# Kernel tuning notes

Measured on AMD Instinct MI355X. Metric: run time of the kernel, lower is better.

The kernel has to match this reference:

```python
import jax, jax.numpy as jnp
import numpy as np

B, N, C = 32, 1025, 768
H, D = 12, 64          # num_heads, head_dim
M = 4 * D              # num random features = 256
HEIGHT, WIDTH = 32, 32 # spatial grid; N = HEIGHT*WIDTH + 1 (CLS)
EPS = 1e-6


def setup_inputs() -> dict:
    key = jax.random.key(0)
    ks = jax.random.split(key, 7)
    x = jax.random.normal(ks[0], (B, N, C), jnp.float32)
    w_qkv = jax.random.normal(ks[1], (3 * C, C), jnp.float32) * 0.02
    w_proj = jax.random.normal(ks[2], (C, C), jnp.float32) * 0.02
    b_proj = jnp.zeros((C,), jnp.float32)
    c_row = jax.random.normal(ks[3], (H, D), jnp.float32) * 0.02
    c_col = jax.random.normal(ks[4], (H, D), jnp.float32) * 0.02
    # orthogonal random-feature projection (m, d): QR blocks scaled by chi norm
    blocks = []
    for i in range(M // D):
        Hm = jax.random.normal(jax.random.fold_in(ks[5], i), (D, D), jnp.float32)
        Q, _ = jnp.linalg.qr(Hm)
        nrm = jnp.linalg.norm(jax.random.normal(jax.random.fold_in(ks[6], i), (D,), jnp.float32))
        blocks.append(Q * nrm)
    proj_feat = jnp.concatenate(blocks, axis=0)  # (M, D)
    return {"x": x, "w_qkv": w_qkv, "w_proj": w_proj, "b_proj": b_proj,
            "c_row": c_row, "c_col": c_col, "proj_feat": proj_feat}


def _string(xp, c_row, c_col):
    """Circulant-STRING rotation. xp: (B,H,Np,D)."""
    rows = jnp.arange(HEIGHT, dtype=jnp.float32)
    cols = jnp.arange(WIDTH, dtype=jnp.float32)
    gr, gc = jnp.meshgrid(rows, cols, indexing='ij')
    pos_r = gr.ravel()  # (Np,)
    pos_c = gc.ravel()
    # g: (H, Np, D)
    g = pos_r[None, :, None] * c_row[:, None, :] + pos_c[None, :, None] * c_col[:, None, :]
    g_fft = jnp.fft.fft(g, axis=-1)
    exp_lambda = jnp.exp(2j * g_fft.imag)          # (H, Np, D) complex, unit modulus
    x_fft = jnp.fft.fft(xp, axis=-1)               # (B, H, Np, D) complex
    rotated = jnp.fft.ifft(exp_lambda[None] * x_fft, axis=-1).real
    return rotated.astype(xp.dtype)


def _favor(x, proj):
    """Positive random feature map. x: (B,H,N,D), proj: (M,D) -> (B,H,N,M)."""
    xs = x * (D ** -0.25)
    px = jnp.einsum('bhnd,md->bhnm', xs, proj)
    norm_sq = 0.5 * jnp.sum(xs * xs, axis=-1, keepdims=True)
    return jnp.exp(px - norm_sq)


def reference(x, w_qkv, w_proj, b_proj, c_row, c_col, proj_feat):
    qkv = x @ w_qkv.T                                  # (B, N, 3C)
    qkv = qkv.reshape(B, N, 3, H, D).transpose(2, 0, 3, 1, 4)  # (3,B,H,N,D)
    q, k, v = qkv[0], qkv[1], qkv[2]
    # N == HEIGHT*WIDTH + 1 -> CLS token at position 0 is left unrotated
    q_cls, q_p = q[:, :, :1, :], q[:, :, 1:, :]
    k_cls, k_p = k[:, :, :1, :], k[:, :, 1:, :]
    q = jnp.concatenate([q_cls, _string(q_p, c_row, c_col)], axis=2)
    k = jnp.concatenate([k_cls, _string(k_p, c_row, c_col)], axis=2)
    q_feat = _favor(q, proj_feat)                      # (B,H,N,M)
    k_feat = _favor(k, proj_feat)
    # bidirectional linear attention
    context = jnp.einsum('bhnm,bhne->bhme', k_feat, v) # (B,H,M,D)
    num = jnp.einsum('bhnm,bhme->bhne', q_feat, context)
    k_sum = k_feat.sum(axis=2)                         # (B,H,M)
    den = jnp.einsum('bhnm,bhm->bhn', q_feat, k_sum)[..., None]
    den = jnp.maximum(den, EPS)
    out = num / den                                    # (B,H,N,D)
    out = out.transpose(0, 2, 1, 3).reshape(B, N, C)
    return out @ w_proj.T + b_proj
```

## Files before the change

kernel.cpp:

```cpp
#include <hip/hip_runtime.h>
#include <math.h>

typedef _Float16 f16;
typedef _Float16 f16x8 __attribute__((ext_vector_type(8)));
typedef _Float16 f16x4 __attribute__((ext_vector_type(4)));
typedef float f32x4 __attribute__((ext_vector_type(4)));

#define LDSK 40
#define NTOK 1025
#define CC 768
#define HH 12
#define DD 64
#define MM 256
#define VPAD 1056
#define BN_ROWS 32800

__device__ __forceinline__ void load_row16(const f16* p, f16x8& a0, f16x8& a1) {
    a0 = *(const f16x8*)p;
    a1 = *(const f16x8*)(p + 8);
}
__device__ __forceinline__ void load_row16(const float* p, f16x8& a0, f16x8& a1) {
    const float4* q = (const float4*)p;
    float4 u0 = q[0], u1 = q[1], u2 = q[2], u3 = q[3];
    a0[0] = (f16)u0.x; a0[1] = (f16)u0.y; a0[2] = (f16)u0.z; a0[3] = (f16)u0.w;
    a0[4] = (f16)u1.x; a0[5] = (f16)u1.y; a0[6] = (f16)u1.z; a0[7] = (f16)u1.w;
    a1[0] = (f16)u2.x; a1[1] = (f16)u2.y; a1[2] = (f16)u2.z; a1[3] = (f16)u2.w;
    a1[4] = (f16)u3.x; a1[5] = (f16)u3.y; a1[6] = (f16)u3.z; a1[7] = (f16)u3.w;
}

__device__ __forceinline__ void gload16(const f16* g, f16* l) {
    __builtin_amdgcn_global_load_lds(
        (const __attribute__((address_space(1))) unsigned int*)g,
        (__attribute__((address_space(3))) unsigned int*)l, 16, 0, 0);
}

__global__ void k_diag(float* out, float v) {
    if (threadIdx.x == 0 && blockIdx.x == 0) out[0] = v;
}

__global__ __launch_bounds__(256) void k_cvt_x(const float* __restrict__ x, f16* __restrict__ xw) {
    size_t i = ((size_t)blockIdx.x * 256 + threadIdx.x) * 4;
    float4 v;
    if (i < (size_t)BN_ROWS * CC) v = *(const float4*)(x + i);
    else v = make_float4(0.f, 0.f, 0.f, 0.f);
    f16x4 o; o[0] = (f16)v.x; o[1] = (f16)v.y; o[2] = (f16)v.z; o[3] = (f16)v.w;
    *(f16x4*)(xw + i) = o;
}

__global__ __launch_bounds__(256) void k_cvt(const float* __restrict__ in, f16* __restrict__ out,
                                             long n, float scale) {
    long i = (long)blockIdx.x * 256 + threadIdx.x;
    if (i < n) out[i] = (f16)(in[i] * scale);
}

__global__ __launch_bounds__(256) void k_zpad(f16* __restrict__ v16t) {
    int bh = blockIdx.x;
    for (int u = threadIdx.x; u < 64 * 31; u += 256) {
        int d = u / 31, j = u - d * 31;
        v16t[((size_t)bh * DD + d) * VPAD + 1025 + j] = (f16)0.f;
    }
}

__global__ __launch_bounds__(64) void k_ab(const float* __restrict__ c_row,
                                           const float* __restrict__ c_col,
                                           float* __restrict__ ab) {
    int h = blockIdx.x, k = threadIdx.x;
    float sa = 0.f, sb = 0.f;
    for (int d = 0; d < 64; ++d) {
        float s = sinf((float)((k * d) & 63) * (6.283185307179586f / 64.f));
        sa += c_row[h * 64 + d] * s;
        sb += c_col[h * 64 + d] * s;
    }
    ab[h * 64 + k] = -2.f * sa;
    ab[768 + h * 64 + k] = -2.f * sb;
}

__global__ __launch_bounds__(64) void k_wcirc(const float* __restrict__ ab, float* __restrict__ wc) {
    int hp = blockIdx.x; int h = hp >> 10; int p = hp & 1023;
    float pr = (float)(p >> 5), pc = (float)(p & 31);
    int t = threadIdx.x;
    __shared__ float th[64];
    th[t] = pr * ab[h * 64 + t] + pc * ab[768 + h * 64 + t];
    __syncthreads();
    float s = 0.f;
    #pragma unroll 8
    for (int k = 0; k < 64; ++k) {
        float arg = th[k] + (float)((k * t) & 63) * (6.283185307179586f / 64.f);
        s += __cosf(arg);
    }
    wc[(size_t)hp * 64 + t] = s * (1.f / 64.f);
}

template <bool GA, typename TA, typename TB>
__device__ __forceinline__ void gemm128_core(const TA* __restrict__ A, const TB* __restrict__ Bm,
                                             int K, int row0, int col0, int Alim,
                                             f32x4 (&acc)[4][4],
                                             f16 (*As)[LDSK], f16 (*Bs)[LDSK]) {
    const int tid = threadIdx.x;
    const int lane = tid & 63;
    const int lr = tid >> 1, lk = (tid & 1) * 16;
    const int frow = lane & 15, fk = (lane >> 4) * 8;
    const int wave = tid >> 6, wr = wave >> 1, wc = wave & 1;
    for (int kt = 0; kt < K; kt += 32) {
        f16x8 a0 = {}, a1 = {}, b0, b1;
        if (!GA || (row0 + lr) < Alim)
            load_row16(A + (size_t)(row0 + lr) * K + kt + lk, a0, a1);
        load_row16(Bm + (size_t)(col0 + lr) * K + kt + lk, b0, b1);
        __syncthreads();
        *(f16x8*)&As[lr][lk] = a0; *(f16x8*)&As[lr][lk + 8] = a1;
        *(f16x8*)&Bs[lr][lk] = b0; *(f16x8*)&Bs[lr][lk + 8] = b1;
        __syncthreads();
        f16x8 af[4], bf[4];
        #pragma unroll
        for (int m = 0; m < 4; ++m) af[m] = *(const f16x8*)&As[wr * 64 + m * 16 + frow][fk];
        #pragma unroll
        for (int n = 0; n < 4; ++n) bf[n] = *(const f16x8*)&Bs[wc * 64 + n * 16 + frow][fk];
        #pragma unroll
        for (int m = 0; m < 4; ++m)
            #pragma unroll
            for (int n = 0; n < 4; ++n)
                acc[m][n] = __builtin_amdgcn_mfma_f32_16x16x32_f16(af[m], bf[n], acc[m][n], 0, 0, 0);
    }
}

__device__ __forceinline__ void gemm128_pipe(const f16* __restrict__ A, const f16* __restrict__ Bm,
                                             int K, int row0, int col0,
                                             f32x4 (&acc)[4][4], f16* As, f16* Bs) {
    const int tid = threadIdx.x;
    const int lane = tid & 63, wave = tid >> 6;
    const int frow = lane & 15, fk8 = (lane >> 4) * 8;
    const int wr = wave >> 1, wc = wave & 1;
    const int srow = lane >> 3;
    const int scol = ((lane & 7) ^ srow) * 8;
    const f16* aG = A + (size_t)(row0 + wave * 32 + srow) * K + scol;
    const f16* bG = Bm + (size_t)(col0 + wave * 32 + srow) * K + scol;
    const int aoff = (wave * 32) * 64;
    const int cswz = (frow & 7) * 8;
    #pragma unroll
    for (int j = 0; j < 4; ++j) {
        gload16(aG + (size_t)(8 * j) * K, As + aoff + (8 * j) * 64);
        gload16(bG + (size_t)(8 * j) * K, Bs + aoff + (8 * j) * 64);
    }
    int cur = 0;
    for (int kt = 0; kt < K; kt += 64) {
        asm volatile("s_waitcnt vmcnt(0)" ::: "memory");
        __builtin_amdgcn_s_barrier();
        asm volatile("" ::: "memory");
        if (kt + 64 < K) {
            int nb = (cur ^ 1) * 8192;
            #pragma unroll
            for (int j = 0; j < 4; ++j) {
                gload16(aG + kt + 64 + (size_t)(8 * j) * K, As + nb + aoff + (8 * j) * 64);
                gload16(bG + kt + 64 + (size_t)(8 * j) * K, Bs + nb + aoff + (8 * j) * 64);
            }
        }
        const f16* Ac = As + cur * 8192;
        const f16* Bc = Bs + cur * 8192;
        #pragma unroll
        for (int ks = 0; ks < 2; ++ks) {
            f16x8 af[4], bf[4];
            #pragma unroll
            for (int m = 0; m < 4; ++m)
                af[m] = *(const f16x8*)&Ac[(wr * 64 + m * 16 + frow) * 64 + ((ks * 32 + fk8) ^ cswz)];
            #pragma unroll
            for (int n = 0; n < 4; ++n)
                bf[n] = *(const f16x8*)&Bc[(wc * 64 + n * 16 + frow) * 64 + ((ks * 32 + fk8) ^ cswz)];
            #pragma unroll
            for (int m = 0; m < 4; ++m)
                #pragma unroll
                for (int n = 0; n < 4; ++n)
                    acc[m][n] = __builtin_amdgcn_mfma_f32_16x16x32_f16(af[m], bf[n], acc[m][n], 0, 0, 0);
        }
        cur ^= 1;
    }
}

__device__ __forceinline__ void qkv_epilogue(f32x4 (&acc)[4][4], int row0, int col0,
                                             f16* __restrict__ q16, f16* __restrict__ k16,
                                             f16* __restrict__ v16t) {
    int lane = threadIdx.x & 63, wave = threadIdx.x >> 6;
    int wr = wave >> 1, wc = wave & 1;
    int rb = row0 + wr * 64 + 4 * (lane >> 4);
    int cb = col0 + wc * 64 + (lane & 15);
    #pragma unroll
    for (int m = 0; m < 4; ++m)
        #pragma unroll
        for (int n = 0; n < 4; ++n)
            #pragma unroll
            for (int i = 0; i < 4; ++i) {
                int r = rb + m * 16 + i;
                if (r >= BN_ROWS) continue;
                int j = cb + n * 16;
                int b = r / NTOK, nn = r - b * NTOK;
                int t = j / CC, rem = j - t * CC;
                int h = rem >> 6, d = rem & 63;
                size_t bh = (size_t)b * HH + h;
                f16 val = (f16)acc[m][n][i];
                if (t == 0) q16[(bh * NTOK + nn) * DD + d] = val;
                else if (t == 1) k16[(bh * NTOK + nn) * DD + d] = val;
                else v16t[(bh * DD + d) * VPAD + nn] = val;
            }
}

__global__ __launch_bounds__(256) void k_gemm_qkv_dma(const f16* __restrict__ A, const f16* __restrict__ Bm,
                                                      f16* __restrict__ q16, f16* __restrict__ k16,
                                                      f16* __restrict__ v16t) {
    __shared__ __attribute__((aligned(16))) f16 As[2 * 128 * 64];
    __shared__ __attribute__((aligned(16))) f16 Bs[2 * 128 * 64];
    const int q = 578, r = 2;
    int xg = blockIdx.x & 7, o8 = blockIdx.x >> 3;
    int wg = (xg < r ? xg * (q + 1) : r * (q + 1) + (xg - r) * q) + o8;
    int row0 = (wg / 18) * 128, col0 = (wg % 18) * 128;
    f32x4 acc[4][4] = {};
    gemm128_pipe(A, Bm, CC, row0, col0, acc, As, Bs);
    qkv_epilogue(acc, row0, col0, q16, k16, v16t);
}

__global__ __launch_bounds__(256) void k_gemm_qkv_f32(const float* __restrict__ A, const f16* __restrict__ Bm,
                                                      f16* __restrict__ q16, f16* __restrict__ k16,
                                                      f16* __restrict__ v16t) {
    __shared__ __attribute__((aligned(16))) f16 As[128][LDSK];
    __shared__ __attribute__((aligned(16))) f16 Bs[128][LDSK];
    f32x4 acc[4][4] = {};
    int row0 = blockIdx.x * 128, col0 = blockIdx.y * 128;
    gemm128_core<true>(A, Bm, CC, row0, col0, BN_ROWS, acc, As, Bs);
    qkv_epilogue(acc, row0, col0, q16, k16, v16t);
}

__global__ __launch_bounds__(256) void k_rotate(const float* __restrict__ wcirc,
                                                f16* __restrict__ q16, f16* __restrict__ k16,
                                                float* __restrict__ nsqq, float* __restrict__ nsqk) {
    const int p = blockIdx.x, h = blockIdx.y;
    const int nn = p + 1;
    const int tid = threadIdx.x;
    __shared__ float wl[64];
    __shared__ __attribute__((aligned(16))) f16 Ws[64][72];
    __shared__ __attribute__((aligned(16))) f16 Xs[64][72];
    if (tid < 64) wl[tid] = wcirc[((size_t)h * 1024 + p) * 64 + tid];
    {
        const int row = tid >> 2;
        const int ch = (tid & 3) * 16;
        const int b = row & 31;
        const f16* src = ((row < 32) ? q16 : k16) + (((size_t)b * HH + h) * NTOK + nn) * DD + ch;
        f16x8 v0 = *(const f16x8*)src;
        f16x8 v1 = *(const f16x8*)(src + 8);
        *(f16x8*)&Xs[row][ch] = v0;
        *(f16x8*)&Xs[row][ch + 8] = v1;
    }
    __syncthreads();
    #pragma unroll
    for (int j = 0; j < 16; ++j) {
        int idx = tid * 16 + j;
        int d = idx >> 6, m = idx & 63;
        Ws[d][m] = (f16)wl[(d - m) & 63];
    }
    __syncthreads();
    const int lane = tid & 63, wave = tid >> 6;
    const int frow = lane & 15, fk = (lane >> 4) * 8;
    f32x4 acc[4] = {};
    #pragma unroll
    for (int kt = 0; kt < 64; kt += 32) {
        f16x8 a = *(const f16x8*)&Xs[wave * 16 + frow][kt + fk];
        #pragma unroll
        for (int n = 0; n < 4; ++n) {
            f16x8 bfr = *(const f16x8*)&Ws[n * 16 + frow][kt + fk];
            acc[n] = __builtin_amdgcn_mfma_f32_16x16x32_f16(a, bfr, acc[n], 0, 0, 0);
        }
    }
    #pragma unroll
    for (int i = 0; i < 4; ++i) {
        int row = wave * 16 + 4 * (lane >> 4) + i;
        int b = row & 31;
        f16* dst = ((row < 32) ? q16 : k16) + (((size_t)b * HH + h) * NTOK + nn) * DD;
        float ss = 0.f;
        #pragma unroll
        for (int n = 0; n < 4; ++n) {
            float v = acc[n][i];
            dst[n * 16 + (lane & 15)] = (f16)v;
            ss += v * v;
        }
        ss += __shfl_xor(ss, 1); ss += __shfl_xor(ss, 2);
        ss += __shfl_xor(ss, 4); ss += __shfl_xor(ss, 8);
        if ((lane & 15) == 0) {
            float* nd = (row < 32) ? nsqq : nsqk;
            nd[((size_t)b * HH + h) * NTOK + nn] = ss * (1.f / 16.f);
        }
    }
}

__global__ __launch_bounds__(256) void k_cls_nsq(const f16* __restrict__ q16, const f16* __restrict__ k16,
                                                 float* __restrict__ nsqq, float* __restrict__ nsqk) {
    int gw = (blockIdx.x * 256 + threadIdx.x) >> 6;
    int lane = threadIdx.x & 63;
    int which = gw & 1; int bh = gw >> 1;
    const f16* src = (which ? k16 : q16) + (size_t)bh * NTOK * DD;
    float v = (float)src[lane];
    float ss = v * v;
    for (int off = 1; off < 64; off <<= 1) ss += __shfl_xor(ss, off);
    if (lane == 0) (which ? nsqk : nsqq)[(size_t)bh * NTOK] = ss * (1.f / 16.f);
}

__global__ __launch_bounds__(512) void k_fctx(const f16* __restrict__ k16, const f16* __restrict__ v16t,
                                              const f16* __restrict__ pfeat, const float* __restrict__ nsqk,
                                              f16* __restrict__ ctxT) {
    __shared__ __attribute__((aligned(16))) f16 uLDS[80 * 136];
    f16 (*fts)[LDSK] = (f16(*)[LDSK])uLDS;
    f16 (*cx)[136]   = (f16(*)[136])uLDS;
    const int bh = blockIdx.x;
    const int tid = threadIdx.x;
    const int lane = tid & 63, w = tid >> 6;
    const int frow = lane & 15, fk8 = (lane >> 4) * 8;
    const int m0 = w * 32;
    f16x8 pf[2][2];
    #pragma unroll
    for (int mf = 0; mf < 2; ++mf)
        #pragma unroll
        for (int kf = 0; kf < 2; ++kf)
            pf[mf][kf] = *(const f16x8*)&pfeat[(m0 + mf * 16 + frow) * DD + kf * 32 + fk8];
    const f16* kb_base = k16 + (size_t)bh * NTOK * DD;
    const f16* vb_base = v16t + (size_t)bh * DD * VPAD;
    const float* ns_base = nsqk + (size_t)bh * NTOK;
    auto loadK = [&](f16x8 (&kb)[2][2], int n0) {
        #pragma unroll
        for (int nf = 0; nf < 2; ++nf) {
            int n = n0 + nf * 16 + frow;
            #pragma unroll
            for (int kf = 0; kf < 2; ++kf) {
                f16x8 z = {};
                if (n < NTOK) z = *(const f16x8*)&kb_base[(size_t)n * DD + kf * 32 + fk8];
                kb[nf][kf] = z;
            }
        }
    };
    f32x4 acc[2][5] = {};
    f16x8 kb[2][2];
    loadK(kb, 0);
    for (int n0 = 0; n0 < VPAD; n0 += 32) {
        f16x8 vb[4];
        #pragma unroll
        for (int ef = 0; ef < 4; ++ef)
            vb[ef] = *(const f16x8*)&vb_base[(size_t)(ef * 16 + frow) * VPAD + n0 + fk8];
        f32x4 fa[2][2] = {};
        #pragma unroll
        for (int kf = 0; kf < 2; ++kf)
            #pragma unroll
            for (int mf = 0; mf < 2; ++mf)
                #pragma unroll
                for (int nf = 0; nf < 2; ++nf)
                    fa[mf][nf] = __builtin_amdgcn_mfma_f32_16x16x32_f16(pf[mf][kf], kb[nf][kf], fa[mf][nf], 0, 0, 0);
        f16x8 kbn[2][2];
        loadK(kbn, n0 + 32);
        #pragma unroll
        for (int nf = 0; nf < 2; ++nf) {
            int ncol = n0 + nf * 16 + frow;
            float ns = (ncol < NTOK) ? ns_base[ncol] : 0.f;
            #pragma unroll
            for (int mf = 0; mf < 2; ++mf)
                #pragma unroll
                for (int i = 0; i < 4; ++i) {
                    int mloc = m0 + mf * 16 + 4 * (lane >> 4) + i;
                    float v = (ncol < NTOK) ? fminf(__expf(fa[mf][nf][i] - ns), 60000.f) : 0.f;
                    fts[mloc][nf * 16 + frow] = (f16)v;
                }
        }
        __syncthreads();
        f16x8 afr[2];
        #pragma unroll
        for (int mf = 0; mf < 2; ++mf) afr[mf] = *(const f16x8*)&fts[m0 + mf * 16 + frow][fk8];
        #pragma unroll
        for (int ef = 0; ef < 4; ++ef)
            #pragma unroll
            for (int mf = 0; mf < 2; ++mf)
                acc[mf][ef] = __builtin_amdgcn_mfma_f32_16x16x32_f16(afr[mf], vb[ef], acc[mf][ef], 0, 0, 0);
        {
            f16x8 bfr;
            #pragma unroll
            for (int j = 0; j < 8; ++j)
                bfr[j] = (f16)((frow == 0 && (n0 + fk8 + j) < NTOK) ? 1.f : 0.f);
            #pragma unroll
            for (int mf = 0; mf < 2; ++mf)
                acc[mf][4] = __builtin_amdgcn_mfma_f32_16x16x32_f16(afr[mf], bfr, acc[mf][4], 0, 0, 0);
        }
        __syncthreads();
        #pragma unroll
        for (int nf = 0; nf < 2; ++nf)
            #pragma unroll
            for (int kf = 0; kf < 2; ++kf)
                kb[nf][kf] = kbn[nf][kf];
    }
    #pragma unroll
    for (int p = 0; p < 2; ++p) {
        __syncthreads();
        if ((w >> 2) == p) {
            int mb = m0 - p * 128;
            #pragma unroll
            for (int mf = 0; mf < 2; ++mf)
                #pragma unroll
                for (int ef = 0; ef < 5; ++ef) {
                    int e = ef * 16 + frow;
                    f16x4 pk;
                    #pragma unroll
                    for (int i = 0; i < 4; ++i) pk[i] = (f16)acc[mf][ef][i];
                    *(f16x4*)&cx[e][mb + mf * 16 + 4 * (lane >> 4)] = pk;
                }
        }
        __syncthreads();
        for (int u = tid; u < 80 * 16; u += 512) {
            int e = u >> 4, seg = u & 15;
            *(f16x8*)&ctxT[((size_t)bh * 80 + e) * MM + p * 128 + seg * 8] =
                *(const f16x8*)&cx[e][seg * 8];
        }
    }
}

__global__ __launch_bounds__(256) void k_fnum(const f16* __restrict__ q16, const f16* __restrict__ pfeat,
                                              const float* __restrict__ nsqq, const f16* __restrict__ ctxT,
                                              f16* __restrict__ attn) {
    __shared__ __attribute__((aligned(16))) f16 qf_s[128][72];
    const int bh = blockIdx.y;
    const int b = bh / HH, h = bh - b * HH;
    const int t0 = blockIdx.x * 128;
    const int tid = threadIdx.x;
    const int lane = tid & 63, w = tid >> 6;
    const int frow = lane & 15, fk8 = (lane >> 4) * 8;
    const f16* qbase = q16 + (size_t)bh * NTOK * DD;
    const f16* cbase = ctxT + (size_t)bh * 80 * MM;
    f16x8 qa[2][2];
    float ns[2][4];
    #pragma unroll
    for (int tf = 0; tf < 2; ++tf) {
        int t = t0 + w * 32 + tf * 16 + frow;
        #pragma unroll
        for (int kf = 0; kf < 2; ++kf) {
            f16x8 z = {};
            if (t < NTOK) z = *(const f16x8*)&qbase[(size_t)t * DD + kf * 32 + fk8];
            qa[tf][kf] = z;
        }
        #pragma unroll
        for (int i = 0; i < 4; ++i) {
            int tr = t0 + w * 32 + tf * 16 + 4 * (lane >> 4) + i;
            ns[tf][i] = (tr < NTOK) ? nsqq[(size_t)bh * NTOK + tr] : 0.f;
        }
    }
    auto loadPB = [&](f16x8 (&pb)[2][2], int mc) {
        #pragma unroll
        for (int nf = 0; nf < 2; ++nf)
            #pragma unroll
            for (int kf = 0; kf < 2; ++kf)
                pb[nf][kf] = *(const f16x8*)&pfeat[(mc * 32 + nf * 16 + frow) * DD + kf * 32 + fk8];
    };
    f32x4 acc[2][5] = {};
    f16x8 pb[2][2];
    loadPB(pb, 0);
    #pragma unroll
    for (int mc = 0; mc < 8; ++mc) {
        f32x4 fa[2][2] = {};
        #pragma unroll
        for (int kf = 0; kf < 2; ++kf)
            #pragma unroll
            for (int tf = 0; tf < 2; ++tf)
                #pragma unroll
                for (int nf = 0; nf < 2; ++nf)
                    fa[tf][nf] = __builtin_amdgcn_mfma_f32_16x16x32_f16(qa[tf][kf], pb[nf][kf], fa[tf][nf], 0, 0, 0);
        f16x8 pbn[2][2];
        loadPB(pbn, (mc + 1) & 7);
        #pragma unroll
        for (int tf = 0; tf < 2; ++tf)
            #pragma unroll
            for (int nf = 0; nf < 2; ++nf)
                #pragma unroll
                for (int i = 0; i < 4; ++i) {
                    int tl = w * 32 + tf * 16 + 4 * (lane >> 4) + i;
                    float v = fminf(__expf(fa[tf][nf][i] - ns[tf][i]), 60000.f);
                    qf_s[tl][nf * 16 + frow] = (f16)v;
                }
        __syncthreads();
        f16x8 afr[2];
        #pragma unroll
        for (int tf = 0; tf < 2; ++tf) afr[tf] = *(const f16x8*)&qf_s[w * 32 + tf * 16 + frow][fk8];
        #pragma unroll
        for (int ef = 0; ef < 5; ++ef) {
            f16x8 bfr = *(const f16x8*)&cbase[(size_t)(ef * 16 + frow) * MM + mc * 32 + fk8];
            #pragma unroll
            for (int tf = 0; tf < 2; ++tf)
                acc[tf][ef] = __builtin_amdgcn_mfma_f32_16x16x32_f16(afr[tf], bfr, acc[tf][ef], 0, 0, 0);
        }
        __syncthreads();
        #pragma unroll
        for (int nf = 0; nf < 2; ++nf)
            #pragma unroll
            for (int kf = 0; kf < 2; ++kf)
                pb[nf][kf] = pbn[nf][kf];
    }
    #pragma unroll
    for (int tf = 0; tf < 2; ++tf)
        #pragma unroll
        for (int i = 0; i < 4; ++i) {
            float den = fmaxf(__shfl(acc[tf][4][i], lane & 48), 1e-6f);
            int tl = w * 32 + tf * 16 + 4 * (lane >> 4) + i;
            #pragma unroll
            for (int ef = 0; ef < 4; ++ef)
                qf_s[tl][ef * 16 + frow] = (f16)(acc[tf][ef][i] / den);
        }
    __syncthreads();
    for (int u = tid; u < 128 * 8; u += 256) {
        int tok = u >> 3, seg = u & 7;
        if (t0 + tok < NTOK)
            *(f16x8*)&attn[((size_t)(b * NTOK + t0 + tok)) * CC + h * DD + seg * 8] =
                *(const f16x8*)&qf_s[tok][seg * 8];
    }
}

__device__ __forceinline__ void proj_epilogue(f32x4 (&acc)[4][4], int row0, int col0,
                                              const float* __restrict__ bias, float* __restrict__ out) {
    int lane = threadIdx.x & 63, wave = threadIdx.x >> 6;
    int wr = wave >> 1, wc = wave & 1;
    int rb = row0 + wr * 64 + 4 * (lane >> 4);
    int cb = col0 + wc * 64 + (lane & 15);
    #pragma unroll
    for (int n = 0; n < 4; ++n) {
        int j = cb + n * 16;
        float bj = bias[j];
        #pragma unroll
        for (int m = 0; m < 4; ++m)
            #pragma unroll
            for (int i = 0; i < 4; ++i) {
                int r = rb + m * 16 + i;
                if (r < BN_ROWS) out[(size_t)r * CC + j] = acc[m][n][i] + bj;
            }
    }
}

__global__ __launch_bounds__(256) void k_gemm_proj_dma(const f16* __restrict__ A, const f16* __restrict__ Bm,
                                                       const float* __restrict__ bias, float* __restrict__ out) {
    __shared__ __attribute__((aligned(16))) f16 As[2 * 128 * 64];
    __shared__ __attribute__((aligned(16))) f16 Bs[2 * 128 * 64];
    const int q = 192, r = 6;
    int xg = blockIdx.x & 7, o8 = blockIdx.x >> 3;
    int wg = (xg < r ? xg * (q + 1) : r * (q + 1) + (xg - r) * q) + o8;
    int row0 = (wg / 6) * 128, col0 = (wg % 6) * 128;
    f32x4 acc[4][4] = {};
    gemm128_pipe(A, Bm, CC, row0, col0, acc, As, Bs);
    proj_epilogue(acc, row0, col0, bias, out);
}

__global__ __launch_bounds__(256) void k_gemm_proj(const f16* __restrict__ A, const f16* __restrict__ Bm,
                                                   const float* __restrict__ bias, float* __restrict__ out) {
    __shared__ __attribute__((aligned(16))) f16 As[128][LDSK];
    __shared__ __attribute__((aligned(16))) f16 Bs[128][LDSK];
    f32x4 acc[4][4] = {};
    int row0 = blockIdx.x * 128, col0 = blockIdx.y * 128;
    gemm128_core<true>(A, Bm, CC, row0, col0, BN_ROWS, acc, As, Bs);
    proj_epilogue(acc, row0, col0, bias, out);
}

extern "C" void kernel_launch(void* const* d_in, const int* in_sizes, int n_in,
                              void* d_out, int out_size, void* d_ws, size_t ws_size,
                              hipStream_t stream) {
    const float* x = (const float*)d_in[0];
    const float* w_qkv = (const float*)d_in[1];
    const float* w_proj = (const float*)d_in[2];
    const float* b_proj = (const float*)d_in[3];
    const float* c_row = (const float*)d_in[4];
    const float* c_col = (const float*)d_in[5];
    const float* proj_feat = (const float*)d_in[6];
    float* out = (float*)d_out;
    char* ws = (char*)d_ws;
    char* ob = (char*)d_out;

    const size_t O_WQKV  = 0;
    const size_t O_WPROJ = 3538944;
    const size_t O_Q16   = 4718592;
    const size_t O_K16   = 55099392;
    const size_t O_XW    = 105480192;
    const size_t NEED_B  = 105480192;
    const size_t NEED_A  = 156008448;
    if (ws_size < NEED_B) {
        k_diag<<<1, 64, 0, stream>>>(out, (float)((double)ws_size / 1048576.0));
        return;
    }
    const bool useA = (ws_size >= NEED_A);

    const size_t OD_V    = 0;
    const size_t OD_CTX  = 51904512;
    const size_t OD_WC   = 67633152;
    const size_t OD_NSQQ = 70778880;
    const size_t OD_NSQK = 72353280;
    const size_t OD_PF   = 73927680;
    const size_t OD_AB   = 73960448;

    f16* wqkv16  = (f16*)(ws + O_WQKV);
    f16* wproj16 = (f16*)(ws + O_WPROJ);
    f16* q16     = (f16*)(ws + O_Q16);
    f16* k16     = (f16*)(ws + O_K16);
    f16* xw16    = (f16*)(ws + O_XW);
    f16* v16t    = (f16*)(ob + OD_V);
    f16* ctxT    = (f16*)(ob + OD_CTX);
    float* wcirc = (float*)(ob + OD_WC);
    float* nsqq  = (float*)(ob + OD_NSQQ);
    float* nsqk  = (float*)(ob + OD_NSQK);
    f16* pfeat16 = (f16*)(ob + OD_PF);
    float* ab    = (float*)(ob + OD_AB);
    f16* attn16  = k16;

    k_cvt<<<6912, 256, 0, stream>>>(w_qkv, wqkv16, 1769472L, 1.f);
    k_cvt<<<2304, 256, 0, stream>>>(w_proj, wproj16, 589824L, 1.f);
    k_cvt<<<64, 256, 0, stream>>>(proj_feat, pfeat16, 16384L, 0.3535533906f);
    k_ab<<<12, 64, 0, stream>>>(c_row, c_col, ab);
    k_wcirc<<<12288, 64, 0, stream>>>(ab, wcirc);

    if (useA) {
        k_cvt_x<<<24672, 256, 0, stream>>>(x, xw16);
        k_gemm_qkv_dma<<<4626, 256, 0, stream>>>(xw16, wqkv16, q16, k16, v16t);
    } else {
        k_gemm_qkv_f32<<<dim3(257, 18), 256, 0, stream>>>(x, wqkv16, q16, k16, v16t);
    }
    k_zpad<<<384, 256, 0, stream>>>(v16t);

    k_rotate<<<dim3(1024, 12), 256, 0, stream>>>(wcirc, q16, k16, nsqq, nsqk);
    k_cls_nsq<<<192, 256, 0, stream>>>(q16, k16, nsqq, nsqk);

    k_fctx<<<384, 512, 0, stream>>>(k16, v16t, pfeat16, nsqk, ctxT);
    k_fnum<<<dim3(9, 384), 256, 0, stream>>>(q16, pfeat16, nsqq, ctxT, attn16);

    if (useA) {
        k_gemm_proj_dma<<<1542, 256, 0, stream>>>(attn16, wproj16, b_proj, out);
    } else {
        k_gemm_proj<<<dim3(257, 6), 256, 0, stream>>>(attn16, wproj16, b_proj, out);
    }

    (void)in_sizes; (void)n_in; (void)out_size;
}
```

Before: 658.8 us.

## Enlarge QKV and projection GEMM tiles to 256x256 with 512-thread blocks

Replaces the 128x128 pipelined GEMM with a 256x256-tile version using 8 waves per block, each wave computing 128x64 with an 8x4 MFMA accumulator array. K is fixed at 768 and the loop is fully specialised, with out-of-range A rows clamped instead of padded. Larger tiles raise arithmetic intensity and cut global/LDS traffic per FLOP, but use 128KB of LDS and more registers, which limits occupancy and makes the last row tile more wasteful. The epilogues are restructured to compute head/type indexing once per lane.

```diff
diff --git a/kernel.cpp b/kernel.cpp
--- a/kernel.cpp
+++ b/kernel.cpp
@@ -123,56 +123,132 @@
     }
 }
 
-__device__ __forceinline__ void gemm128_pipe(const f16* __restrict__ A, const f16* __restrict__ Bm,
-                                             int K, int row0, int col0,
-                                             f32x4 (&acc)[4][4], f16* As, f16* Bs) {
+__device__ __forceinline__ void gemm256_pipe(const f16* __restrict__ A, const f16* __restrict__ Bm,
+                                             int row0, int col0, int aclamp,
+                                             f32x4 (&acc)[8][4], f16* As, f16* Bs) {
     const int tid = threadIdx.x;
-    const int lane = tid & 63, wave = tid >> 6;
-    const int frow = lane & 15, fk8 = (lane >> 4) * 8;
-    const int wr = wave >> 1, wc = wave & 1;
+    const int lane = tid & 63, w = tid >> 6;
+    const int frow = lane & 15;
     const int srow = lane >> 3;
-    const int scol = ((lane & 7) ^ srow) * 8;
-    const f16* aG = A + (size_t)(row0 + wave * 32 + srow) * K + scol;
-    const f16* bG = Bm + (size_t)(col0 + wave * 32 + srow) * K + scol;
-    const int aoff = (wave * 32) * 64;
+    const int schk = ((lane & 7) ^ srow) * 8;
+    const f16* aG[4]; const f16* bG[4];
+    f16* aL[4]; f16* bL[4];
+    #pragma unroll
+    for (int j = 0; j < 4; ++j) {
+        int ra = row0 + w * 32 + 8 * j + srow;
+        if (ra > aclamp) ra = aclamp;
+        aG[j] = A + (size_t)ra * CC + schk;
+        bG[j] = Bm + (size_t)(col0 + w * 32 + 8 * j + srow) * CC + schk;
+        aL[j] = As + (w * 32 + 8 * j) * 64;
+        bL[j] = Bs + (w * 32 + 8 * j) * 64;
+    }
+    auto STAGE = [&](int tt) {
+        int bo = (tt & 1) * 16384, ko = tt * 64;
+        #pragma unroll
+        for (int j = 0; j < 4; ++j) {
+            gload16(aG[j] + ko, aL[j] + bo);
+            gload16(bG[j] + ko, bL[j] + bo);
+        }
+    };
+    STAGE(0);
+    const int wr = w >> 2, wcn = w & 3;
+    const int fk8 = (lane >> 4) * 8;
     const int cswz = (frow & 7) * 8;
-    #pragma unroll
-    for (int j = 0; j < 4; ++j) {
-        gload16(aG + (size_t)(8 * j) * K, As + aoff + (8 * j) * 64);
-        gload16(bG + (size_t)(8 * j) * K, Bs + aoff + (8 * j) * 64);
-    }
-    int cur = 0;
-    for (int kt = 0; kt < K; kt += 64) {
+    for (int t = 0; t < 12; ++t) {
         asm volatile("s_waitcnt vmcnt(0)" ::: "memory");
         __builtin_amdgcn_s_barrier();
-        asm volatile("" ::: "memory");
-        if (kt + 64 < K) {
-            int nb = (cur ^ 1) * 8192;
-            #pragma unroll
-            for (int j = 0; j < 4; ++j) {
-                gload16(aG + kt + 64 + (size_t)(8 * j) * K, As + nb + aoff + (8 * j) * 64);
-                gload16(bG + kt + 64 + (size_t)(8 * j) * K, Bs + nb + aoff + (8 * j) * 64);
+        __builtin_amdgcn_sched_barrier(0);
+        if (t < 11) STAGE(t + 1);
+        const f16* Ac = As + (t & 1) * 16384;
+        const f16* Bc = Bs + (t & 1) * 16384;
+        #pragma unroll
+        for (int ks = 0; ks < 2; ++ks) {
+            const int co = (ks * 32 + fk8) ^ cswz;
+            f16x8 af[8], bf[4];
+            #pragma unroll
+            for (int n = 0; n < 4; ++n)
+                bf[n] = *(const f16x8*)&Bc[(wcn * 64 + n * 16 + frow) * 64 + co];
+            #pragma unroll
+            for (int m = 0; m < 8; ++m)
+                af[m] = *(const f16x8*)&Ac[(wr * 128 + m * 16 + frow) * 64 + co];
+            #pragma unroll
+            for (int n = 0; n < 4; ++n)
+                #pragma unroll
+                for (int m = 0; m < 8; ++m)
+                    acc[m][n] = __builtin_amdgcn_mfma_f32_16x16x32_f16(af[m], bf[n], acc[m][n], 0, 0, 0);
+        }
+    }
+}
+
+__global__ __launch_bounds__(512, 2) void k_gemm_qkv_256(const f16* __restrict__ A, const f16* __restrict__ Bm,
+                                                         f16* __restrict__ q16, f16* __restrict__ k16,
+                                                         f16* __restrict__ v16t) {
+    __shared__ __attribute__((aligned(16))) f16 As[2 * 256 * 64];
+    __shared__ __attribute__((aligned(16))) f16 Bs[2 * 256 * 64];
+    const int q = 145, r = 1;
+    int xg = blockIdx.x & 7, o8 = blockIdx.x >> 3;
+    int wg = (xg < r ? xg * (q + 1) : r * (q + 1) + (xg - r) * q) + o8;
+    int row0 = (wg / 9) * 256, col0 = (wg % 9) * 256;
+    f32x4 acc[8][4] = {};
+    gemm256_pipe(A, Bm, row0, col0, 32895, acc, As, Bs);
+    const int lane = threadIdx.x & 63, w = threadIdx.x >> 6;
+    const int wr = w >> 2, wcn = w & 3;
+    int cb = col0 + wcn * 64 + (lane & 15);
+    int tt = cb / CC;
+    int h = (cb - tt * CC) >> 6;
+    int d0 = lane & 15;
+    int rb = row0 + wr * 128 + 4 * (lane >> 4);
+    #pragma unroll
+    for (int m = 0; m < 8; ++m)
+        #pragma unroll
+        for (int i = 0; i < 4; ++i) {
+            int rr = rb + m * 16 + i;
+            if (rr >= BN_ROWS) continue;
+            int b = rr / NTOK, nn = rr - b * NTOK;
+            size_t bh = (size_t)b * HH + h;
+            if (tt == 0) {
+                f16* p = q16 + (bh * NTOK + nn) * DD + d0;
+                #pragma unroll
+                for (int n = 0; n < 4; ++n) p[n * 16] = (f16)acc[m][n][i];
+            } else if (tt == 1) {
+                f16* p = k16 + (bh * NTOK + nn) * DD + d0;
+                #pragma unroll
+                for (int n = 0; n < 4; ++n) p[n * 16] = (f16)acc[m][n][i];
+            } else {
+                f16* p = v16t + (bh * DD + d0) * VPAD + nn;
+                #pragma unroll
+                for (int n = 0; n < 4; ++n) p[(size_t)n * 16 * VPAD] = (f16)acc[m][n][i];
             }
         }
-        const f16* Ac = As + cur * 8192;
-        const f16* Bc = Bs + cur * 8192;
-        #pragma unroll
-        for (int ks = 0; ks < 2; ++ks) {
-            f16x8 af[4], bf[4];
-            #pragma unroll
-            for (int m = 0; m < 4; ++m)
-                af[m] = *(const f16x8*)&Ac[(wr * 64 + m * 16 + frow) * 64 + ((ks * 32 + fk8) ^ cswz)];
-            #pragma unroll
-            for (int n = 0; n < 4; ++n)
-                bf[n] = *(const f16x8*)&Bc[(wc * 64 + n * 16 + frow) * 64 + ((ks * 32 + fk8) ^ cswz)];
-            #pragma unroll
-            for (int m = 0; m < 4; ++m)
-                #pragma unroll
-                for (int n = 0; n < 4; ++n)
-                    acc[m][n] = __builtin_amdgcn_mfma_f32_16x16x32_f16(af[m], bf[n], acc[m][n], 0, 0, 0);
-        }
-        cur ^= 1;
-    }
+}
+
+__global__ __launch_bounds__(512, 2) void k_gemm_proj_256(const f16* __restrict__ A, const f16* __restrict__ Bm,
+                                                          const float* __restrict__ bias, float* __restrict__ out) {
+    __shared__ __attribute__((aligned(16))) f16 As[2 * 256 * 64];
+    __shared__ __attribute__((aligned(16))) f16 Bs[2 * 256 * 64];
+    const int q = 48, r = 3;
+    int xg = blockIdx.x & 7, o8 = blockIdx.x >> 3;
+    int wg = (xg < r ? xg * (q + 1) : r * (q + 1) + (xg - r) * q) + o8;
+    int row0 = (wg / 3) * 256, col0 = (wg % 3) * 256;
+    f32x4 acc[8][4] = {};
+    gemm256_pipe(A, Bm, row0, col0, 32799, acc, As, Bs);
+    const int lane = threadIdx.x & 63, w = threadIdx.x >> 6;
+    const int wr = w >> 2, wcn = w & 3;
+    int cb = col0 + wcn * 64 + (lane & 15);
+    float bj[4];
+    #pragma unroll
+    for (int n = 0; n < 4; ++n) bj[n] = bias[cb + n * 16];
+    int rb = row0 + wr * 128 + 4 * (lane >> 4);
+    #pragma unroll
+    for (int m = 0; m < 8; ++m)
+        #pragma unroll
+        for (int i = 0; i < 4; ++i) {
+            int rr = rb + m * 16 + i;
+            if (rr >= BN_ROWS) continue;
+            float* p = out + (size_t)rr * CC + cb;
+            #pragma unroll
+            for (int n = 0; n < 4; ++n) p[n * 16] = acc[m][n][i] + bj[n];
+        }
 }
 
 __device__ __forceinline__ void qkv_epilogue(f32x4 (&acc)[4][4], int row0, int col0,
@@ -200,20 +276,6 @@
                 else if (t == 1) k16[(bh * NTOK + nn) * DD + d] = val;
                 else v16t[(bh * DD + d) * VPAD + nn] = val;
             }
-}
-
-__global__ __launch_bounds__(256) void k_gemm_qkv_dma(const f16* __restrict__ A, const f16* __restrict__ Bm,
-                                                      f16* __restrict__ q16, f16* __restrict__ k16,
-                                                      f16* __restrict__ v16t) {
-    __shared__ __attribute__((aligned(16))) f16 As[2 * 128 * 64];
-    __shared__ __attribute__((aligned(16))) f16 Bs[2 * 128 * 64];
-    const int q = 578, r = 2;
-    int xg = blockIdx.x & 7, o8 = blockIdx.x >> 3;
-    int wg = (xg < r ? xg * (q + 1) : r * (q + 1) + (xg - r) * q) + o8;
-    int row0 = (wg / 18) * 128, col0 = (wg % 18) * 128;
-    f32x4 acc[4][4] = {};
-    gemm128_pipe(A, Bm, CC, row0, col0, acc, As, Bs);
-    qkv_epilogue(acc, row0, col0, q16, k16, v16t);
 }
 
 __global__ __launch_bounds__(256) void k_gemm_qkv_f32(const float* __restrict__ A, const f16* __restrict__ Bm,
@@ -531,19 +593,6 @@
     }
 }
 
-__global__ __launch_bounds__(256) void k_gemm_proj_dma(const f16* __restrict__ A, const f16* __restrict__ Bm,
-                                                       const float* __restrict__ bias, float* __restrict__ out) {
-    __shared__ __attribute__((aligned(16))) f16 As[2 * 128 * 64];
-    __shared__ __attribute__((aligned(16))) f16 Bs[2 * 128 * 64];
-    const int q = 192, r = 6;
-    int xg = blockIdx.x & 7, o8 = blockIdx.x >> 3;
-    int wg = (xg < r ? xg * (q + 1) : r * (q + 1) + (xg - r) * q) + o8;
-    int row0 = (wg / 6) * 128, col0 = (wg % 6) * 128;
-    f32x4 acc[4][4] = {};
-    gemm128_pipe(A, Bm, CC, row0, col0, acc, As, Bs);
-    proj_epilogue(acc, row0, col0, bias, out);
-}
-
 __global__ __launch_bounds__(256) void k_gemm_proj(const f16* __restrict__ A, const f16* __restrict__ Bm,
                                                    const float* __restrict__ bias, float* __restrict__ out) {
     __shared__ __attribute__((aligned(16))) f16 As[128][LDSK];
@@ -611,7 +660,7 @@
 
     if (useA) {
         k_cvt_x<<<24672, 256, 0, stream>>>(x, xw16);
-        k_gemm_qkv_dma<<<4626, 256, 0, stream>>>(xw16, wqkv16, q16, k16, v16t);
+        k_gemm_qkv_256<<<1161, 512, 0, stream>>>(xw16, wqkv16, q16, k16, v16t);
     } else {
         k_gemm_qkv_f32<<<dim3(257, 18), 256, 0, stream>>>(x, wqkv16, q16, k16, v16t);
     }
@@ -624,7 +673,7 @@
     k_fnum<<<dim3(9, 384), 256, 0, stream>>>(q16, pfeat16, nsqq, ctxT, attn16);
 
     if (useA) {
-        k_gemm_proj_dma<<<1542, 256, 0, stream>>>(attn16, wproj16, b_proj, out);
+        k_gemm_proj_256<<<387, 512, 0, stream>>>(attn16, wproj16, b_proj, out);
     } else {
         k_gemm_proj<<<dim3(257, 6), 256, 0, stream>>>(attn16, wproj16, b_proj, out);
     }
```

New measurement: 644.7 us. 2.1% less time.
